# Performance work log

Hardware: AMD Instinct MI355X
Metric: run time of the kernel (lower is better)

Reference implementation:

```python
import jax, jax.numpy as jnp
import numpy as np

N, E = 50000, 800000
F_IN, HID, HEADS, OUT = 128, 32, 4, 16
NEG_SLOPE = 0.2  # PyG GATConv default leaky_relu slope


def segment_softmax(logits, seg, n):
    # numerically stable softmax over edges grouped by destination node
    m = jax.ops.segment_max(logits, seg, num_segments=n)          # [N,H]
    m = jnp.where(jnp.isfinite(m), m, 0.0)                        # guard empty segments
    e = jnp.exp(logits - m[seg])                                  # [E,H]
    s = jax.ops.segment_sum(e, seg, num_segments=n)               # [N,H]
    return e / (s[seg] + 1e-16)


def gat_conv(x, W, a_src, a_dst, bias, src, dst, concat):
    H, C = a_src.shape
    n = x.shape[0]
    h = (x @ W).reshape(n, H, C)                                  # [N,H,C]
    alpha_src = jnp.einsum('nhc,hc->nh', h, a_src)                # [N,H]
    alpha_dst = jnp.einsum('nhc,hc->nh', h, a_dst)                # [N,H]
    e = jax.nn.leaky_relu(alpha_src[src] + alpha_dst[dst], NEG_SLOPE)  # [E,H]
    alpha = segment_softmax(e, dst, n)                            # [E,H]
    msg = h[src] * alpha[:, :, None]                              # [E,H,C]
    out = jax.ops.segment_sum(msg, dst, num_segments=n)           # [N,H,C]
    out = out.reshape(n, H * C) if concat else out.mean(axis=1)
    return out + bias


def setup_inputs() -> dict:
    key = jax.random.key(0)
    ks = jax.random.split(key, 12)
    s = 0.1  # keep attention logits in a sane range
    return {
        'x': jax.random.normal(ks[0], (N, F_IN), jnp.float32),
        'edge_index': jax.random.randint(ks[1], (2, E), 0, N),
        'Wemb': jax.random.normal(ks[2], (F_IN, HID), jnp.float32) * s,
        'bemb': jnp.zeros((HID,), jnp.float32),
        'W1': jax.random.normal(ks[3], (HID, HEADS * HID), jnp.float32) * s,
        'a_src1': jax.random.normal(ks[4], (HEADS, HID), jnp.float32) * s,
        'a_dst1': jax.random.normal(ks[5], (HEADS, HID), jnp.float32) * s,
        'b1': jnp.zeros((HEADS * HID,), jnp.float32),
        'W2': jax.random.normal(ks[6], (HEADS * HID, HEADS * OUT), jnp.float32) * s,
        'a_src2': jax.random.normal(ks[7], (HEADS, OUT), jnp.float32) * s,
        'a_dst2': jax.random.normal(ks[8], (HEADS, OUT), jnp.float32) * s,
        'b2': jnp.zeros((OUT,), jnp.float32),
    }


def reference(x, edge_index, Wemb, bemb, W1, a_src1, a_dst1, b1, W2, a_src2, a_dst2, b2):
    src, dst = edge_index[0], edge_index[1]
    h = x @ Wemb + bemb  # dropout layers are identity at inference
    h = jax.nn.elu(gat_conv(h, W1, a_src1, a_dst1, b1, src, dst, True))
    h = gat_conv(h, W2, a_src2, a_dst2, b2, src, dst, False)
    return jax.nn.log_softmax(h, axis=1)
```

## Files before the change

### kernel.cpp

```cpp
#include <hip/hip_runtime.h>

#define N_NODES 50000
#define N_EDGES 800000
#define F_IN    128
#define HID     32
#define HEADS   4
#define OUT_C   16

#define NBKT 196
#define CAP  5120
#define EPB  4096
#define NB64 782

__device__ __forceinline__ unsigned short f2bf(float f) {
    unsigned int u = __float_as_uint(f);
    u += 0x7FFFu + ((u >> 16) & 1u);
    return (unsigned short)(u >> 16);
}
__device__ __forceinline__ float bf_lo(unsigned int u) { return __uint_as_float(u << 16); }
__device__ __forceinline__ float bf_hi(unsigned int u) { return __uint_as_float(u & 0xFFFF0000u); }
__device__ __forceinline__ float bf2f(unsigned short s) {
    return __uint_as_float(((unsigned int)s) << 16);
}

__device__ __forceinline__ float edge_w(float asv, float adv) {
    float v = asv + adv;
    v = (v > 0.f) ? v : 0.2f * v;
    return __expf(v);
}

__global__ __launch_bounds__(256) void k_F1(const float* __restrict__ x,
                                            const float* __restrict__ Wemb,
                                            const float* __restrict__ bemb,
                                            float* __restrict__ h0,
                                            const int* __restrict__ ei,
                                            int* __restrict__ gcnt,
                                            unsigned int* __restrict__ pairs) {
    __shared__ float xs[64][132];
    __shared__ float Wl[F_IN][HID];
    __shared__ float bl[HID];
    __shared__ int hist[NBKT];
    __shared__ int base[NBKT];
    int t = threadIdx.x;
    if (blockIdx.x < NB64) {
        int node0 = blockIdx.x * 64;
        if (t < HID) bl[t] = bemb[t];
        #pragma unroll
        for (int it = 0; it < 4; it++) {
            int idx = it * 256 + t;
            *(float4*)((float*)Wl + idx * 4) = *(const float4*)(Wemb + idx * 4);
        }
        #pragma unroll
        for (int it = 0; it < 8; it++) {
            int idx = it * 256 + t;
            int row = idx >> 5, c4 = idx & 31;
            float4 v = make_float4(0.f, 0.f, 0.f, 0.f);
            if (node0 + row < N_NODES) v = *(const float4*)(x + (size_t)(node0 + row) * F_IN + c4 * 4);
            *(float4*)&xs[row][c4 * 4] = v;
        }
        __syncthreads();
        int c = t & 7, g = t >> 3;
        float acc[2][4] = {};
        for (int k = 0; k < F_IN; k++) {
            float4 w4 = *(const float4*)&Wl[k][c * 4];
            #pragma unroll
            for (int n = 0; n < 2; n++) {
                float xv = xs[g * 2 + n][k];
                acc[n][0] += xv * w4.x; acc[n][1] += xv * w4.y;
                acc[n][2] += xv * w4.z; acc[n][3] += xv * w4.w;
            }
        }
        #pragma unroll
        for (int n = 0; n < 2; n++) {
            int node = node0 + g * 2 + n;
            if (node < N_NODES) {
                float4 o = make_float4(acc[n][0] + bl[c * 4], acc[n][1] + bl[c * 4 + 1],
                                       acc[n][2] + bl[c * 4 + 2], acc[n][3] + bl[c * 4 + 3]);
                *(float4*)(h0 + (size_t)node * HID + c * 4) = o;
            }
        }
    } else {
        int e0 = (blockIdx.x - NB64) * EPB;
        for (int i = t; i < NBKT; i += 256) hist[i] = 0;
        __syncthreads();
        unsigned int p[16];
        int bb[16];
        #pragma unroll
        for (int i = 0; i < 16; i++) {
            int e = e0 + i * 256 + t;
            bb[i] = -1;
            if (e < N_EDGES) {
                int s = ei[e], d = ei[N_EDGES + e];
                p[i] = ((unsigned int)s << 8) | (unsigned int)(d & 255);
                bb[i] = d >> 8;
                atomicAdd(&hist[bb[i]], 1);
            }
        }
        __syncthreads();
        for (int i = t; i < NBKT; i += 256) {
            int c = hist[i];
            base[i] = i * CAP + (c ? atomicAdd(&gcnt[i], c) : 0);
            hist[i] = 0;
        }
        __syncthreads();
        #pragma unroll
        for (int i = 0; i < 16; i++) {
            if (bb[i] >= 0) {
                int off = atomicAdd(&hist[bb[i]], 1);
                pairs[base[bb[i]] + off] = p[i];
            }
        }
    }
}

__global__ __launch_bounds__(256) void k_F2(const float* __restrict__ h0,
                                            const float* __restrict__ W1,
                                            const float* __restrict__ a_src,
                                            const float* __restrict__ a_dst,
                                            unsigned short* __restrict__ h1,
                                            float* __restrict__ as, float* __restrict__ ad,
                                            const unsigned int* __restrict__ pairs,
                                            const int* __restrict__ gcnt,
                                            int* __restrict__ rowptr,
                                            int* __restrict__ esrc) {
    __shared__ float xs[64][36];
    __shared__ float Wl[HID][128];
    __shared__ int cnt[256];
    __shared__ int cur[256];
    __shared__ int wsum[4];
    int t = threadIdx.x;
    if (blockIdx.x < NB64) {
        int node0 = blockIdx.x * 64;
        #pragma unroll
        for (int it = 0; it < 4; it++) {
            int idx = it * 256 + t;
            *(float4*)((float*)Wl + idx * 4) = *(const float4*)(W1 + idx * 4);
        }
        #pragma unroll
        for (int it = 0; it < 2; it++) {
            int idx = it * 256 + t;
            int row = idx >> 3, c4 = idx & 7;
            float4 v = make_float4(0.f, 0.f, 0.f, 0.f);
            if (node0 + row < N_NODES) v = *(const float4*)(h0 + (size_t)(node0 + row) * HID + c4 * 4);
            *(float4*)&xs[row][c4 * 4] = v;
        }
        __syncthreads();
        int c = t & 31, g = t >> 5;
        float acc[8][4] = {};
        for (int k = 0; k < HID; k++) {
            float4 w4 = *(const float4*)&Wl[k][c * 4];
            #pragma unroll
            for (int n = 0; n < 8; n++) {
                float xv = xs[g * 8 + n][k];
                acc[n][0] += xv * w4.x; acc[n][1] += xv * w4.y;
                acc[n][2] += xv * w4.z; acc[n][3] += xv * w4.w;
            }
        }
        float4 av = *(const float4*)(a_src + c * 4);
        float4 dv = *(const float4*)(a_dst + c * 4);
        float ps[8], pd[8];
        #pragma unroll
        for (int n = 0; n < 8; n++) {
            int node = node0 + g * 8 + n;
            if (node < N_NODES) {
                ushort4 o;
                o.x = f2bf(acc[n][0]); o.y = f2bf(acc[n][1]);
                o.z = f2bf(acc[n][2]); o.w = f2bf(acc[n][3]);
                *(ushort4*)(h1 + (size_t)node * 128 + c * 4) = o;
            }
            ps[n] = acc[n][0] * av.x + acc[n][1] * av.y + acc[n][2] * av.z + acc[n][3] * av.w;
            pd[n] = acc[n][0] * dv.x + acc[n][1] * dv.y + acc[n][2] * dv.z + acc[n][3] * dv.w;
        }
        #pragma unroll
        for (int mask = 1; mask <= 4; mask <<= 1) {
            #pragma unroll
            for (int n = 0; n < 8; n++) {
                ps[n] += __shfl_xor(ps[n], mask, 64);
                pd[n] += __shfl_xor(pd[n], mask, 64);
            }
        }
        if ((c & 7) == 0) {
            int hh = c >> 3;
            #pragma unroll
            for (int n = 0; n < 8; n++) {
                int node = node0 + g * 8 + n;
                if (node < N_NODES) { as[node * 4 + hh] = ps[n]; ad[node * 4 + hh] = pd[n]; }
            }
        }
    } else {
        int b = blockIdx.x - NB64;
        int lane = t & 63, wv = t >> 6;
        int v0 = (t < NBKT && t < b) ? gcnt[t] : 0;
        #pragma unroll
        for (int mask = 1; mask < 64; mask <<= 1) v0 += __shfl_xor(v0, mask, 64);
        if (lane == 0) wsum[wv] = v0;
        __syncthreads();
        int base = wsum[0] + wsum[1] + wsum[2] + wsum[3];
        int n0 = b << 8;
        int cntb = gcnt[b];
        int s0 = b * CAP;
        cnt[t] = 0;
        __syncthreads();
        for (int i = t; i < cntb; i += 256) atomicAdd(&cnt[pairs[s0 + i] & 255], 1);
        __syncthreads();
        int v = cnt[t], x = v;
        #pragma unroll
        for (int off = 1; off < 64; off <<= 1) { int y = __shfl_up(x, off, 64); if (lane >= off) x += y; }
        __syncthreads();
        if (lane == 63) wsum[wv] = x;
        __syncthreads();
        int add = 0;
        for (int j = 0; j < wv; j++) add += wsum[j];
        int excl = base + (x - v) + add;
        cur[t] = excl;
        if (n0 + t < N_NODES) rowptr[n0 + t] = excl;
        if (b == 0 && t == 0) rowptr[N_NODES] = N_EDGES;
        __syncthreads();
        for (int i = t; i < cntb; i += 256) {
            unsigned int p = pairs[s0 + i];
            int pos = atomicAdd(&cur[p & 255], 1);
            esrc[pos] = (int)(p >> 8);
        }
    }
}

__global__ __launch_bounds__(256) void k_h2f(const unsigned int* __restrict__ hin,
                                             const float* __restrict__ W2,
                                             const float* __restrict__ a_src,
                                             const float* __restrict__ a_dst,
                                             unsigned short* __restrict__ h2,
                                             float* __restrict__ as, float* __restrict__ ad) {
    __shared__ float xs[64][132];
    __shared__ float Wl[128][64];
    int t = threadIdx.x;
    int node0 = blockIdx.x * 64;
    #pragma unroll
    for (int it = 0; it < 8; it++) {
        int idx = it * 256 + t;
        *(float4*)((float*)Wl + idx * 4) = *(const float4*)(W2 + idx * 4);
    }
    #pragma unroll
    for (int it = 0; it < 8; it++) {
        int idx = it * 256 + t;
        int row = idx >> 5, c4 = idx & 31;
        float4 v = make_float4(0.f, 0.f, 0.f, 0.f);
        if (node0 + row < N_NODES) {
            uint2 u = *(const uint2*)(hin + (size_t)(node0 + row) * 64 + c4 * 2);
            v = make_float4(bf_lo(u.x), bf_hi(u.x), bf_lo(u.y), bf_hi(u.y));
        }
        *(float4*)&xs[row][c4 * 4] = v;
    }
    __syncthreads();
    int c = t & 15, g = t >> 4;
    float acc[4][4] = {};
    for (int k = 0; k < 128; k++) {
        float4 w4 = *(const float4*)&Wl[k][c * 4];
        #pragma unroll
        for (int n = 0; n < 4; n++) {
            float xv = xs[g * 4 + n][k];
            acc[n][0] += xv * w4.x; acc[n][1] += xv * w4.y;
            acc[n][2] += xv * w4.z; acc[n][3] += xv * w4.w;
        }
    }
    float4 av = *(const float4*)(a_src + c * 4);
    float4 dv = *(const float4*)(a_dst + c * 4);
    float ps[4], pd[4];
    #pragma unroll
    for (int n = 0; n < 4; n++) {
        int node = node0 + g * 4 + n;
        if (node < N_NODES) {
            ushort4 o;
            o.x = f2bf(acc[n][0]); o.y = f2bf(acc[n][1]);
            o.z = f2bf(acc[n][2]); o.w = f2bf(acc[n][3]);
            *(ushort4*)(h2 + (size_t)node * 64 + c * 4) = o;
        }
        ps[n] = acc[n][0] * av.x + acc[n][1] * av.y + acc[n][2] * av.z + acc[n][3] * av.w;
        pd[n] = acc[n][0] * dv.x + acc[n][1] * dv.y + acc[n][2] * dv.z + acc[n][3] * dv.w;
    }
    #pragma unroll
    for (int mask = 1; mask <= 2; mask <<= 1) {
        #pragma unroll
        for (int n = 0; n < 4; n++) {
            ps[n] += __shfl_xor(ps[n], mask, 64);
            pd[n] += __shfl_xor(pd[n], mask, 64);
        }
    }
    if ((c & 3) == 0) {
        int hh = c >> 2;
        #pragma unroll
        for (int n = 0; n < 4; n++) {
            int node = node0 + g * 4 + n;
            if (node < N_NODES) { as[node * 4 + hh] = ps[n]; ad[node * 4 + hh] = pd[n]; }
        }
    }
}

__global__ __launch_bounds__(256) void k_gather1(const int* __restrict__ esrc,
                                                 const int* __restrict__ rowptr,
                                                 const unsigned int* __restrict__ h1,
                                                 const float* __restrict__ as,
                                                 const float* __restrict__ ad,
                                                 const float* __restrict__ b1,
                                                 unsigned int* __restrict__ out1) {
    int t = threadIdx.x;
    int node = blockIdx.x * 4 + (t >> 6);
    int lane = t & 63;
    int head = lane >> 4;
    int s16 = lane >> 2;
    int h4 = lane & 3;
    int lb = lane * 4;
    int hb = head * 4;
    int beg = rowptr[node], end = rowptr[node + 1];
    float ad_w = ad[node * 4 + h4];
    float ax = 0.f, ay = 0.f, s = 0.f;
    const char* h1c = (const char*)h1;
    for (int k = beg; k < end; k += 16) {
        int idx = k + s16;
        int sm = esrc[min(idx, end - 1)];
#define G1L(J) int sj##J = __builtin_amdgcn_readlane(sm, (J) * 4); \
        unsigned int u##J = *(const unsigned int*)(h1c + (size_t)(unsigned)sj##J * 256 + lb);
        G1L(0)  G1L(1)  G1L(2)  G1L(3)  G1L(4)  G1L(5)  G1L(6)  G1L(7)
        G1L(8)  G1L(9)  G1L(10) G1L(11) G1L(12) G1L(13) G1L(14) G1L(15)
#undef G1L
        float wm = edge_w(as[sm * 4 + h4], ad_w);
        if (idx >= end) wm = 0.f;
        int wmi = __float_as_int(wm);
#define G1W(J) float w##J = __int_as_float(__builtin_amdgcn_ds_bpermute(hb + (J) * 16, wmi));
        G1W(0)  G1W(1)  G1W(2)  G1W(3)  G1W(4)  G1W(5)  G1W(6)  G1W(7)
        G1W(8)  G1W(9)  G1W(10) G1W(11) G1W(12) G1W(13) G1W(14) G1W(15)
#undef G1W
        ax += bf_lo(u0)  * w0  + bf_lo(u1)  * w1  + bf_lo(u2)  * w2  + bf_lo(u3)  * w3
            + bf_lo(u4)  * w4  + bf_lo(u5)  * w5  + bf_lo(u6)  * w6  + bf_lo(u7)  * w7
            + bf_lo(u8)  * w8  + bf_lo(u9)  * w9  + bf_lo(u10) * w10 + bf_lo(u11) * w11
            + bf_lo(u12) * w12 + bf_lo(u13) * w13 + bf_lo(u14) * w14 + bf_lo(u15) * w15;
        ay += bf_hi(u0)  * w0  + bf_hi(u1)  * w1  + bf_hi(u2)  * w2  + bf_hi(u3)  * w3
            + bf_hi(u4)  * w4  + bf_hi(u5)  * w5  + bf_hi(u6)  * w6  + bf_hi(u7)  * w7
            + bf_hi(u8)  * w8  + bf_hi(u9)  * w9  + bf_hi(u10) * w10 + bf_hi(u11) * w11
            + bf_hi(u12) * w12 + bf_hi(u13) * w13 + bf_hi(u14) * w14 + bf_hi(u15) * w15;
        s += (w0 + w1 + w2 + w3) + (w4 + w5 + w6 + w7)
           + (w8 + w9 + w10 + w11) + (w12 + w13 + w14 + w15);
    }
    float rs = 1.0f / (s + 1e-16f);
    float2 bv = *(const float2*)(b1 + 2 * lane);
    float vx = ax * rs + bv.x;
    float vy = ay * rs + bv.y;
    vx = (vx > 0.f) ? vx : (__expf(vx) - 1.0f);
    vy = (vy > 0.f) ? vy : (__expf(vy) - 1.0f);
    out1[(size_t)node * 64 + lane] = ((unsigned int)f2bf(vy) << 16) | (unsigned int)f2bf(vx);
}

__global__ __launch_bounds__(256) void k_gather2(const int* __restrict__ esrc,
                                                 const int* __restrict__ rowptr,
                                                 const unsigned short* __restrict__ h2,
                                                 const float* __restrict__ as,
                                                 const float* __restrict__ ad,
                                                 const float* __restrict__ b2,
                                                 float* __restrict__ out) {
    int t = threadIdx.x;
    int node = blockIdx.x * 4 + (t >> 6);
    int lane = t & 63;
    int head = lane >> 4, c = lane & 15;
    int s16 = lane >> 2;
    int h4 = lane & 3;
    int lb = lane * 2;
    int hb = head * 4;
    int beg = rowptr[node], end = rowptr[node + 1];
    float ad_w = ad[node * 4 + h4];
    float acc = 0.f, s = 0.f;
    const char* h2c = (const char*)h2;
    for (int k = beg; k < end; k += 16) {
        int idx = k + s16;
        int sm = esrc[min(idx, end - 1)];
#define G2L(J) int sj##J = __builtin_amdgcn_readlane(sm, (J) * 4); \
        float r##J = bf2f(*(const unsigned short*)(h2c + (size_t)(unsigned)sj##J * 128 + lb));
        G2L(0)  G2L(1)  G2L(2)  G2L(3)  G2L(4)  G2L(5)  G2L(6)  G2L(7)
        G2L(8)  G2L(9)  G2L(10) G2L(11) G2L(12) G2L(13) G2L(14) G2L(15)
#undef G2L
        float wm = edge_w(as[sm * 4 + h4], ad_w);
        if (idx >= end) wm = 0.f;
        int wmi = __float_as_int(wm);
#define G2W(J) float w##J = __int_as_float(__builtin_amdgcn_ds_bpermute(hb + (J) * 16, wmi));
        G2W(0)  G2W(1)  G2W(2)  G2W(3)  G2W(4)  G2W(5)  G2W(6)  G2W(7)
        G2W(8)  G2W(9)  G2W(10) G2W(11) G2W(12) G2W(13) G2W(14) G2W(15)
#undef G2W
        acc += r0 * w0 + r1 * w1 + r2 * w2 + r3 * w3
             + r4 * w4 + r5 * w5 + r6 * w6 + r7 * w7
             + r8 * w8 + r9 * w9 + r10 * w10 + r11 * w11
             + r12 * w12 + r13 * w13 + r14 * w14 + r15 * w15;
        s += (w0 + w1 + w2 + w3) + (w4 + w5 + w6 + w7)
           + (w8 + w9 + w10 + w11) + (w12 + w13 + w14 + w15);
    }
    float v = acc * (1.0f / (s + 1e-16f));
    v += __shfl_xor(v, 16, 64);
    v += __shfl_xor(v, 32, 64);
    v = v * 0.25f + b2[c];
    float m = v;
    #pragma unroll
    for (int mask = 1; mask < 16; mask <<= 1) m = fmaxf(m, __shfl_xor(m, mask, 64));
    float ex = __expf(v - m);
    float se = ex;
    #pragma unroll
    for (int mask = 1; mask < 16; mask <<= 1) se += __shfl_xor(se, mask, 64);
    float res = (v - m) - __logf(se);
    if (lane < 16) out[(size_t)node * 16 + lane] = res;
}

extern "C" void kernel_launch(void* const* d_in, const int* in_sizes, int n_in,
                              void* d_out, int out_size, void* d_ws, size_t ws_size,
                              hipStream_t stream) {
    const float* x      = (const float*)d_in[0];
    const int*   ei     = (const int*)d_in[1];
    const float* Wemb   = (const float*)d_in[2];
    const float* bemb   = (const float*)d_in[3];
    const float* W1     = (const float*)d_in[4];
    const float* a_src1 = (const float*)d_in[5];
    const float* a_dst1 = (const float*)d_in[6];
    const float* b1     = (const float*)d_in[7];
    const float* W2     = (const float*)d_in[8];
    const float* a_src2 = (const float*)d_in[9];
    const float* a_dst2 = (const float*)d_in[10];
    const float* b2     = (const float*)d_in[11];
    float* out = (float*)d_out;

    char* ws = (char*)d_ws;
    size_t off = 0;
    auto alloc = [&](size_t bytes) { char* p = ws + off; off += (bytes + 255) & ~size_t(255); return p; };
    unsigned short* h1b   = (unsigned short*)alloc((size_t)N_NODES * 128 * 2);
    unsigned int*   out1b = (unsigned int*)alloc((size_t)N_NODES * 64 * 4);
    float*        h0    = (float*)alloc((size_t)N_NODES * HID * 4);
    int*          esrc  = (int*)alloc((size_t)N_EDGES * 4 + 64);
    unsigned int* pairs = (unsigned int*)alloc((size_t)NBKT * CAP * 4);
    float* as     = (float*)alloc((size_t)N_NODES * 4 * 4);
    float* ad     = (float*)alloc((size_t)N_NODES * 4 * 4);
    int*   rowptr = (int*)alloc((size_t)(N_NODES + 1) * 4);
    int*   gcnt   = (int*)alloc((size_t)NBKT * 4);
    unsigned short* h2b = h1b;

    const int GB = N_NODES / 4;

    hipMemsetAsync(gcnt, 0, (size_t)NBKT * 4, stream);
    k_F1<<<NB64 + NBKT, 256, 0, stream>>>(x, Wemb, bemb, h0, ei, gcnt, pairs);
    k_F2<<<NB64 + NBKT, 256, 0, stream>>>(h0, W1, a_src1, a_dst1, h1b, as, ad,
                                          pairs, gcnt, rowptr, esrc);
    k_gather1<<<GB, 256, 0, stream>>>(esrc, rowptr, (const unsigned int*)h1b, as, ad, b1, out1b);
    k_h2f<<<NB64, 256, 0, stream>>>((const unsigned int*)out1b, W2, a_src2, a_dst2, h2b, as, ad);
    k_gather2<<<GB, 256, 0, stream>>>(esrc, rowptr, h2b, as, ad, b2, out);
}
```

Measured before the change: 211.2 us.

## Use bf16 MFMA for layer-2 projection GEMM in k_h2f

Replaces the scalar FP32 FMA loop in the layer-2 linear transform with MFMA 16x16x32 bf16 matrix instructions. The bf16 input rows are kept as bf16 in shared memory, and W2 is converted to bf16 and transposed into shared memory. The attention-logit dot products are computed with 16-lane shuffle reductions. This cuts ALU work and shared-memory traffic for the GEMM, but W2 is now rounded to bf16, which loses some precision, and the reduction uses more shuffles.

```diff
diff --git a/kernel.cpp b/kernel.cpp
--- a/kernel.cpp
+++ b/kernel.cpp
@@ -11,6 +11,9 @@
 #define CAP  5120
 #define EPB  4096
 #define NB64 782
+
+typedef __attribute__((ext_vector_type(8))) short bf16x8;
+typedef __attribute__((ext_vector_type(4))) float f32x4;
 
 __device__ __forceinline__ unsigned short f2bf(float f) {
     unsigned int u = __float_as_uint(f);
@@ -230,67 +233,64 @@
                                              const float* __restrict__ a_dst,
                                              unsigned short* __restrict__ h2,
                                              float* __restrict__ as, float* __restrict__ ad) {
-    __shared__ float xs[64][132];
-    __shared__ float Wl[128][64];
+    __shared__ unsigned int xsu[64][68];
+    __shared__ unsigned short w2t[64][136];
     int t = threadIdx.x;
     int node0 = blockIdx.x * 64;
     #pragma unroll
+    for (int it = 0; it < 4; it++) {
+        int idx = it * 256 + t;
+        int row = idx >> 4, c4 = idx & 15;
+        uint4 v = make_uint4(0u, 0u, 0u, 0u);
+        if (node0 + row < N_NODES) v = *(const uint4*)(hin + (size_t)(node0 + row) * 64 + c4 * 4);
+        *(uint4*)&xsu[row][c4 * 4] = v;
+    }
+    #pragma unroll
     for (int it = 0; it < 8; it++) {
         int idx = it * 256 + t;
-        *(float4*)((float*)Wl + idx * 4) = *(const float4*)(W2 + idx * 4);
-    }
-    #pragma unroll
-    for (int it = 0; it < 8; it++) {
-        int idx = it * 256 + t;
-        int row = idx >> 5, c4 = idx & 31;
-        float4 v = make_float4(0.f, 0.f, 0.f, 0.f);
-        if (node0 + row < N_NODES) {
-            uint2 u = *(const uint2*)(hin + (size_t)(node0 + row) * 64 + c4 * 2);
-            v = make_float4(bf_lo(u.x), bf_hi(u.x), bf_lo(u.y), bf_hi(u.y));
-        }
-        *(float4*)&xs[row][c4 * 4] = v;
+        int k = idx >> 4, n4 = idx & 15;
+        float4 w = *(const float4*)(W2 + k * 64 + n4 * 4);
+        w2t[n4 * 4 + 0][k] = f2bf(w.x);
+        w2t[n4 * 4 + 1][k] = f2bf(w.y);
+        w2t[n4 * 4 + 2][k] = f2bf(w.z);
+        w2t[n4 * 4 + 3][k] = f2bf(w.w);
     }
     __syncthreads();
-    int c = t & 15, g = t >> 4;
-    float acc[4][4] = {};
-    for (int k = 0; k < 128; k++) {
-        float4 w4 = *(const float4*)&Wl[k][c * 4];
-        #pragma unroll
-        for (int n = 0; n < 4; n++) {
-            float xv = xs[g * 4 + n][k];
-            acc[n][0] += xv * w4.x; acc[n][1] += xv * w4.y;
-            acc[n][2] += xv * w4.z; acc[n][3] += xv * w4.w;
-        }
-    }
-    float4 av = *(const float4*)(a_src + c * 4);
-    float4 dv = *(const float4*)(a_dst + c * 4);
-    float ps[4], pd[4];
-    #pragma unroll
-    for (int n = 0; n < 4; n++) {
-        int node = node0 + g * 4 + n;
-        if (node < N_NODES) {
-            ushort4 o;
-            o.x = f2bf(acc[n][0]); o.y = f2bf(acc[n][1]);
-            o.z = f2bf(acc[n][2]); o.w = f2bf(acc[n][3]);
-            *(ushort4*)(h2 + (size_t)node * 64 + c * 4) = o;
-        }
-        ps[n] = acc[n][0] * av.x + acc[n][1] * av.y + acc[n][2] * av.z + acc[n][3] * av.w;
-        pd[n] = acc[n][0] * dv.x + acc[n][1] * dv.y + acc[n][2] * dv.z + acc[n][3] * dv.w;
-    }
-    #pragma unroll
-    for (int mask = 1; mask <= 2; mask <<= 1) {
-        #pragma unroll
-        for (int n = 0; n < 4; n++) {
-            ps[n] += __shfl_xor(ps[n], mask, 64);
-            pd[n] += __shfl_xor(pd[n], mask, 64);
-        }
-    }
-    if ((c & 3) == 0) {
-        int hh = c >> 2;
-        #pragma unroll
-        for (int n = 0; n < 4; n++) {
-            int node = node0 + g * 4 + n;
-            if (node < N_NODES) { as[node * 4 + hh] = ps[n]; ad[node * 4 + hh] = pd[n]; }
+    int lane = t & 63, wv = t >> 6;
+    int lrow = lane & 15, lk = lane >> 4;
+    f32x4 acc[4] = {};
+    const char* xbase = (const char*)&xsu[wv * 16 + lrow][0] + lk * 16;
+    #pragma unroll
+    for (int kt = 0; kt < 4; kt++) {
+        bf16x8 af = *(const bf16x8*)(xbase + kt * 64);
+        #pragma unroll
+        for (int h = 0; h < 4; h++) {
+            bf16x8 bfr = *(const bf16x8*)((const char*)&w2t[h * 16 + lrow][0] + kt * 64 + lk * 16);
+            acc[h] = __builtin_amdgcn_mfma_f32_16x16x32_bf16(af, bfr, acc[h], 0, 0, 0);
+        }
+    }
+    float av[4], dv[4];
+    #pragma unroll
+    for (int h = 0; h < 4; h++) { av[h] = a_src[h * 16 + lrow]; dv[h] = a_dst[h * 16 + lrow]; }
+    #pragma unroll
+    for (int r = 0; r < 4; r++) {
+        int node = node0 + wv * 16 + lk * 4 + r;
+        float psh[4], pdh[4];
+        #pragma unroll
+        for (int h = 0; h < 4; h++) {
+            float v = acc[h][r];
+            if (node < N_NODES) h2[(size_t)node * 64 + h * 16 + lrow] = f2bf(v);
+            float p = v * av[h], q = v * dv[h];
+            #pragma unroll
+            for (int mask = 1; mask < 16; mask <<= 1) {
+                p += __shfl_xor(p, mask, 64);
+                q += __shfl_xor(q, mask, 64);
+            }
+            psh[h] = p; pdh[h] = q;
+        }
+        if (lrow == 0 && node < N_NODES) {
+            *(float4*)(as + node * 4) = make_float4(psh[0], psh[1], psh[2], psh[3]);
+            *(float4*)(ad + node * 4) = make_float4(pdh[0], pdh[1], pdh[2], pdh[3]);
         }
     }
 }
```

Result: faster. 204.1 us (-3.3%).
